# Kernel tuning notes

Hardware: AMD Instinct MI355X
Metric: run time of the kernel (lower is better)

Reference implementation:

```python
import math
import jax, jax.numpy as jnp
import numpy as np

B, S, H = 2, 2048, 1024
NH = 16
HD = H // NH  # 64
THETA = 10000.0


def _rope_cache(seq_len, head_dim, theta):
    inv_freq = 1.0 / (theta ** (jnp.arange(0, head_dim, 2, dtype=jnp.float32) / head_dim))
    pos = jnp.arange(seq_len, dtype=jnp.float32)
    freqs = jnp.outer(pos, inv_freq)           # (S, HD/2)
    emb = jnp.concatenate([freqs, freqs], -1)  # (S, HD)
    return jnp.cos(emb), jnp.sin(emb)


def _apply_rotary(x, cos, sin):
    # x: (B, NH, S, HD); cos/sin: (S, HD) broadcast over B, NH
    d = x.shape[-1] // 2
    x1, x2 = x[..., :d], x[..., d:]
    rotated = jnp.concatenate([-x2, x1], -1)
    return x * cos + rotated * sin


def setup_inputs() -> dict:
    key = jax.random.key(0)
    ks = jax.random.split(key, 5)
    scale = 1.0 / math.sqrt(H)
    return {
        'x': jax.random.normal(ks[0], (B, S, H), jnp.float32),
        'Wq': jax.random.normal(ks[1], (H, H), jnp.float32) * scale,
        'Wk': jax.random.normal(ks[2], (H, H), jnp.float32) * scale,
        'Wv': jax.random.normal(ks[3], (H, H), jnp.float32) * scale,
        'Wo': jax.random.normal(ks[4], (H, H), jnp.float32) * scale,
    }


def reference(x, Wq, Wk, Wv, Wo):
    b, s, h = x.shape
    # projections (nn.Linear: x @ W.T)
    q = (x @ Wq.T).reshape(b, s, NH, HD).transpose(0, 2, 1, 3)
    k = (x @ Wk.T).reshape(b, s, NH, HD).transpose(0, 2, 1, 3)
    v = (x @ Wv.T).reshape(b, s, NH, HD).transpose(0, 2, 1, 3)
    cos, sin = _rope_cache(s, HD, THETA)
    q = _apply_rotary(q, cos, sin)
    k = _apply_rotary(k, cos, sin)
    scale = 1.0 / math.sqrt(HD)
    attn = jnp.einsum('bhqd,bhkd->bhqk', q, k) * scale
    causal = jnp.triu(jnp.ones((s, s), dtype=bool), k=1)
    attn = jnp.where(causal, -jnp.inf, attn)
    attn = jax.nn.softmax(attn, axis=-1)
    out = jnp.einsum('bhqk,bhkd->bhqd', attn, v)
    out = out.transpose(0, 2, 1, 3).reshape(b, s, h)
    return out @ Wo.T
```

## Files before the change

### kernel.cpp

```cpp
#include <hip/hip_runtime.h>

#define B_  2
#define S_  2048
#define H_  1024
#define NH_ 16
#define HD_ 64
#define M_  (B_ * S_)

typedef short  short8  __attribute__((ext_vector_type(8)));
typedef __bf16 bf16x8  __attribute__((ext_vector_type(8)));
typedef float  f32x4   __attribute__((ext_vector_type(4)));

__device__ __forceinline__ ushort f2bf(float f) {
  union { float f; unsigned u; } v; v.f = f;
  unsigned r = v.u + 0x7fffu + ((v.u >> 16) & 1u);
  return (ushort)(r >> 16);
}
__device__ __forceinline__ float bf2f(ushort u) {
  union { unsigned u; float f; } v; v.u = ((unsigned)u) << 16;
  return v.f;
}
__device__ __forceinline__ unsigned cvtpk(float lo, float hi) {
  unsigned r;
  asm("v_cvt_pk_bf16_f32 %0, %1, %2" : "=v"(r) : "v"(lo), "v"(hi));
  return r;
}

__device__ __forceinline__ void gload_lds16(const void* g, void* l) {
  __builtin_amdgcn_global_load_lds(
      (const __attribute__((address_space(1))) void*)g,
      (__attribute__((address_space(3))) void*)l, 16, 0, 0);
}

__device__ __forceinline__ f32x4 mfma_bf16(short8 a, short8 b, f32x4 c) {
  return __builtin_amdgcn_mfma_f32_16x16x32_bf16(
      __builtin_bit_cast(bf16x8, a), __builtin_bit_cast(bf16x8, b), c, 0, 0, 0);
}

__device__ __forceinline__ int swzK(int r, int c) {
  return r * 64 + ((c ^ (r & 7)) << 3);
}
__device__ __forceinline__ int swzV(int r, int c) {
  return r * 128 + ((c ^ (r & 7)) << 3);
}

__device__ __forceinline__ float redmax64(float a) {
  a = fmaxf(a, __shfl_xor(a, 16));
  a = fmaxf(a, __shfl_xor(a, 32));
  return a;
}

__global__ __launch_bounds__(256)
void prep(const float* __restrict__ x, const float* __restrict__ Wq,
          const float* __restrict__ Wk, const float* __restrict__ Wv,
          const float* __restrict__ Wo, ushort* __restrict__ xb,
          ushort* __restrict__ Wqkv, ushort* __restrict__ Wob,
          float* __restrict__ ct, float* __restrict__ st) {
  int bid = blockIdx.x, t = threadIdx.x;
  if (bid < 4096) {
    int i = (bid * 256 + t) * 4;
    float4 v = *(const float4*)&x[i];
    ushort4 o;
    o.x = f2bf(v.x); o.y = f2bf(v.y); o.z = f2bf(v.z); o.w = f2bf(v.w);
    *(ushort4*)&xb[i] = o;
  } else if (bid < 8192) {
    int y = (bid - 4096) >> 10;
    const float* src = (y == 0) ? Wq : (y == 1) ? Wk : (y == 2) ? Wv : Wo;
    ushort* dst = (y == 3) ? Wob : Wqkv + (size_t)y * H_ * H_;
    int i = (((bid - 4096) & 1023) * 256 + t) * 4;
    float4 v = *(const float4*)&src[i];
    ushort4 o;
    o.x = f2bf(v.x); o.y = f2bf(v.y); o.z = f2bf(v.z); o.w = f2bf(v.w);
    *(ushort4*)&dst[i] = o;
  } else {
    int i = (bid - 8192) * 256 + t;
    int pos = i >> 5, d2 = i & 31;
    float invf = powf(10000.0f, -(float)d2 / 32.0f);
    float fr = (float)pos * invf;
    ct[i] = cosf(fr);
    st[i] = sinf(fr);
  }
}

template <int OUT_BF16>
__global__ __launch_bounds__(256)
void gemm_bt(const ushort* __restrict__ A, const ushort* __restrict__ Bm,
             void* __restrict__ Cout, int Mdim, int Ndim, int Kdim) {
  __shared__ ushort As[128 * 64];
  __shared__ ushort Bs[128 * 64];
  int t = threadIdx.x;
  int w = t >> 6, l = t & 63;
  int m0 = blockIdx.y * 128, n0 = blockIdx.x * 128;
  int wr = (w >> 1) * 64, wc = (w & 1) * 64;
  int lrow = l & 15, g = l >> 4;

  f32x4 acc[4][4];
#pragma unroll
  for (int mi = 0; mi < 4; ++mi)
#pragma unroll
    for (int ni = 0; ni < 4; ++ni) acc[mi][ni] = f32x4{0.f, 0.f, 0.f, 0.f};

  for (int k0 = 0; k0 < Kdim; k0 += 64) {
    __syncthreads();
#pragma unroll
    for (int cc = 0; cc < 4; ++cc) {
      int slot = cc * 256 + t;
      int r = slot >> 3, c = slot & 7;
      int cs = (c ^ (r & 7)) << 3;
      gload_lds16(&A[(size_t)(m0 + r) * Kdim + k0 + cs], &As[slot * 8]);
      gload_lds16(&Bm[(size_t)(n0 + r) * Kdim + k0 + cs], &Bs[slot * 8]);
    }
    __syncthreads();
#pragma unroll
    for (int kk = 0; kk < 2; ++kk) {
      short8 af[4], bfr[4];
#pragma unroll
      for (int i = 0; i < 4; ++i)
        af[i] = *(const short8*)&As[swzK(wr + i * 16 + lrow, kk * 4 + g)];
#pragma unroll
      for (int i = 0; i < 4; ++i)
        bfr[i] = *(const short8*)&Bs[swzK(wc + i * 16 + lrow, kk * 4 + g)];
#pragma unroll
      for (int mi = 0; mi < 4; ++mi)
#pragma unroll
        for (int ni = 0; ni < 4; ++ni)
          acc[mi][ni] = mfma_bf16(af[mi], bfr[ni], acc[mi][ni]);
    }
  }

#pragma unroll
  for (int mi = 0; mi < 4; ++mi)
#pragma unroll
    for (int ni = 0; ni < 4; ++ni)
#pragma unroll
      for (int j = 0; j < 4; ++j) {
        int row = m0 + wr + mi * 16 + g * 4 + j;
        int col = n0 + wc + ni * 16 + lrow;
        float vv = acc[mi][ni][j];
        if (OUT_BF16)
          ((ushort*)Cout)[(size_t)row * Ndim + col] = f2bf(vv);
        else
          ((float*)Cout)[(size_t)row * Ndim + col] = vv;
      }
}

__global__ __launch_bounds__(256)
void rope_scatter(const ushort* __restrict__ QKV, const float* __restrict__ ct,
                  const float* __restrict__ st, ushort* __restrict__ qb,
                  ushort* __restrict__ kb) {
  const float SC = 0.125f * 1.44269504f;
  int i = blockIdx.x * 256 + threadIdx.x;
  int row = i >> 9;
  int rem = i & 511;
  int h = rem >> 5, d2 = rem & 31;
  int b = row >> 11, s = row & 2047;
  size_t base = (size_t)row * 3072;
  float c = ct[s * 32 + d2], sn = st[s * 32 + d2];
  size_t o = ((size_t)(b * NH_ + h) * S_ + s) * HD_;

  float x1 = bf2f(QKV[base + h * 64 + d2]);
  float x2 = bf2f(QKV[base + h * 64 + d2 + 32]);
  qb[o + d2]      = f2bf((x1 * c - x2 * sn) * SC);
  qb[o + d2 + 32] = f2bf((x2 * c + x1 * sn) * SC);

  x1 = bf2f(QKV[base + 1024 + h * 64 + d2]);
  x2 = bf2f(QKV[base + 1024 + h * 64 + d2 + 32]);
  kb[o + d2]      = f2bf(x1 * c - x2 * sn);
  kb[o + d2 + 32] = f2bf(x2 * c + x1 * sn);
}

__global__ __launch_bounds__(256)
void transp_v(const ushort* __restrict__ QKV, ushort* __restrict__ vt) {
  __shared__ ushort T[64][72];
  int s0 = blockIdx.x * 64, bh = blockIdx.y;
  int b = bh >> 4, h = bh & 15;
  int t = threadIdx.x;
#pragma unroll
  for (int cc = 0; cc < 2; ++cc) {
    int slot = cc * 256 + t;
    int r = slot >> 3, c = slot & 7;
    short8 v = *(const short8*)
        &QKV[(size_t)(b * S_ + s0 + r) * 3072 + 2048 + h * 64 + c * 8];
#pragma unroll
    for (int i = 0; i < 8; ++i) T[c * 8 + i][r] = (ushort)v[i];
  }
  __syncthreads();
  ushort* dst = vt + (size_t)bh * HD_ * S_;
#pragma unroll
  for (int cc = 0; cc < 2; ++cc) {
    int slot = cc * 256 + t;
    int d = slot >> 3, c = slot & 7;
    *(short8*)&dst[(size_t)d * S_ + s0 + c * 8] = *(const short8*)&T[d][c * 8];
  }
}

__global__ __launch_bounds__(512, 4)
void flash_attn(const ushort* __restrict__ qb, const ushort* __restrict__ kb,
                const ushort* __restrict__ vt, ushort* __restrict__ ctx) {
  __shared__ ushort Ks[128 * 64];
  __shared__ ushort Vs[2][64 * 128];
  __shared__ ushort Ps[128 * 64];
  int bh = blockIdx.y;
  int qt = (blockIdx.y & 16) ? (int)blockIdx.x : (15 - (int)blockIdx.x);
  int b = bh >> 4, h = bh & 15;
  int t = threadIdx.x, w = t >> 6, l = t & 63;
  int lrow = l & 15, g = l >> 4;
  int wrow = w * 16;
  const ushort* Q = qb + (size_t)bh * S_ * HD_;
  const ushort* K = kb + (size_t)bh * S_ * HD_;
  const ushort* V = vt + (size_t)bh * HD_ * S_;

  short8 ones;
#pragma unroll
  for (int i = 0; i < 8; ++i) ones[i] = (short)0x3F80;

#pragma unroll
  for (int cc = 0; cc < 2; ++cc) {
    int slot = cc * 512 + t;
    int r = slot >> 3, c = slot & 7;
    int cs = (c ^ (r & 7)) << 3;
    gload_lds16(&K[(size_t)r * 64 + cs], &Ks[slot * 8]);
  }
#pragma unroll
  for (int cc = 0; cc < 2; ++cc) {
    int slot = cc * 512 + t;
    int r = slot >> 4, c = slot & 15;
    int cs = (c ^ (r & 7)) << 3;
    gload_lds16(&V[(size_t)r * S_ + cs], &Vs[0][slot * 8]);
  }
  short8 aq[2];
  {
    int qrow = qt * 128 + wrow + lrow;
#pragma unroll
    for (int ks = 0; ks < 2; ++ks)
      aq[ks] = *(const short8*)&Q[(size_t)qrow * 64 + ks * 32 + g * 8];
  }
  __syncthreads();

  float m_ = -1e30f, ls_ = 0.f;
  f32x4 O[4];
#pragma unroll
  for (int nf = 0; nf < 4; ++nf) O[nf] = f32x4{0.f, 0.f, 0.f, 0.f};

  int nkt = qt + 1;
  for (int kt = 0; kt < nkt; ++kt) {
    const ushort* Vc = Vs[kt & 1];

    f32x4 sc[8];
#pragma unroll
    for (int nf = 0; nf < 8; ++nf) sc[nf] = f32x4{0.f, 0.f, 0.f, 0.f};
    __builtin_amdgcn_s_setprio(1);
#pragma unroll
    for (int ks = 0; ks < 2; ++ks)
#pragma unroll
      for (int nf = 0; nf < 8; ++nf) {
        short8 bk = *(const short8*)&Ks[swzK(nf * 16 + lrow, ks * 4 + g)];
        sc[nf] = mfma_bf16(bk, aq[ks], sc[nf]);
      }
    __builtin_amdgcn_s_setprio(0);

    __syncthreads();

    if (kt + 1 < nkt) {
      int nb = (kt + 1) & 1;
#pragma unroll
      for (int cc = 0; cc < 2; ++cc) {
        int slot = cc * 512 + t;
        int r = slot >> 3, c = slot & 7;
        int cs = (c ^ (r & 7)) << 3;
        gload_lds16(&K[(size_t)((kt + 1) * 128 + r) * 64 + cs], &Ks[slot * 8]);
      }
#pragma unroll
      for (int cc = 0; cc < 2; ++cc) {
        int slot = cc * 512 + t;
        int r = slot >> 4, c = slot & 15;
        int cs = (c ^ (r & 7)) << 3;
        gload_lds16(&V[(size_t)r * S_ + (kt + 1) * 128 + cs], &Vs[nb][slot * 8]);
      }
    }

    int qbase = qt * 128 + wrow;
    if (kt * 128 + 127 > qbase) {
      int qi = qbase + lrow;
#pragma unroll
      for (int nf = 0; nf < 8; ++nf) {
        int kbase = kt * 128 + nf * 16 + g * 4;
#pragma unroll
        for (int j = 0; j < 4; ++j)
          if (kbase + j > qi) sc[nf][j] = -1e30f;
      }
    }

    f32x4 v4 = sc[0];
#pragma unroll
    for (int nf = 1; nf < 8; ++nf)
#pragma unroll
      for (int j = 0; j < 4; ++j) v4[j] = fmaxf(v4[j], sc[nf][j]);
    float mx = redmax64(fmaxf(fmaxf(v4[0], v4[1]), fmaxf(v4[2], v4[3])));

    bool nor = __all(mx <= m_ + 8.f);
    if (!nor) {
      float mnew = fmaxf(m_, mx);
      float al = exp2f(m_ - mnew);
      m_ = mnew;
      ls_ *= al;
#pragma unroll
      for (int nf = 0; nf < 4; ++nf)
#pragma unroll
        for (int j = 0; j < 4; ++j) O[nf][j] *= al;
    }

#pragma unroll
    for (int nf = 0; nf < 8; ++nf)
#pragma unroll
      for (int j = 0; j < 4; ++j) sc[nf][j] = exp2f(sc[nf][j] - m_);

    f32x4 sacc = f32x4{0.f, 0.f, 0.f, 0.f};
#pragma unroll
    for (int half = 0; half < 2; ++half) {
      int prow = wrow + lrow;
#pragma unroll
      for (int nf2 = 0; nf2 < 4; ++nf2) {
        int nf = half * 4 + nf2;
        uint2 pk;
        pk.x = cvtpk(sc[nf][0], sc[nf][1]);
        pk.y = cvtpk(sc[nf][2], sc[nf][3]);
        *(uint2*)&Ps[swzK(prow, nf2 * 2 + (g >> 1)) + (g & 1) * 4] = pk;
      }
      __builtin_amdgcn_s_setprio(1);
#pragma unroll
      for (int ks2 = 0; ks2 < 2; ++ks2) {
        short8 ap = *(const short8*)&Ps[swzK(wrow + lrow, ks2 * 4 + g)];
        sacc = mfma_bf16(ones, ap, sacc);
#pragma unroll
        for (int nf = 0; nf < 4; ++nf) {
          short8 bv = *(const short8*)&Vc[swzV(nf * 16 + lrow, half * 8 + ks2 * 4 + g)];
          O[nf] = mfma_bf16(bv, ap, O[nf]);
        }
      }
      __builtin_amdgcn_s_setprio(0);
    }
    ls_ += sacc[0];

    __syncthreads();
  }

  float inv = 1.f / ls_;
  int srow = qt * 128 + wrow + lrow;
#pragma unroll
  for (int nf = 0; nf < 4; ++nf) {
    uint2 pk;
    pk.x = cvtpk(O[nf][0] * inv, O[nf][1] * inv);
    pk.y = cvtpk(O[nf][2] * inv, O[nf][3] * inv);
    *(uint2*)&ctx[((size_t)b * S_ + srow) * H_ + h * 64 + nf * 16 + g * 4] = pk;
  }
}

extern "C" void kernel_launch(void* const* d_in, const int* in_sizes, int n_in,
                              void* d_out, int out_size, void* d_ws, size_t ws_size,
                              hipStream_t stream) {
  const float* x  = (const float*)d_in[0];
  const float* Wq = (const float*)d_in[1];
  const float* Wk = (const float*)d_in[2];
  const float* Wv = (const float*)d_in[3];
  const float* Wo = (const float*)d_in[4];

  char* ws = (char*)d_ws;
  size_t off = 0;
  ushort* xb   = (ushort*)(ws + off); off += (size_t)M_ * H_ * 2;
  ushort* Wqkv = (ushort*)(ws + off); off += (size_t)3 * H_ * H_ * 2;
  ushort* Wob  = (ushort*)(ws + off); off += (size_t)H_ * H_ * 2;
  float*  ct   = (float*)(ws + off);  off += (size_t)S_ * 32 * 4;
  float*  st   = (float*)(ws + off);  off += (size_t)S_ * 32 * 4;
  ushort* QKV  = (ushort*)(ws + off); off += (size_t)M_ * 3 * H_ * 2;
  ushort* qb   = (ushort*)(ws + off); off += (size_t)M_ * H_ * 2;
  ushort* kb   = (ushort*)(ws + off); off += (size_t)M_ * H_ * 2;
  ushort* vtb  = (ushort*)(ws + off); off += (size_t)M_ * H_ * 2;
  ushort* ctx  = (ushort*)(ws + off); off += (size_t)M_ * H_ * 2;

  prep<<<8448, 256, 0, stream>>>(x, Wq, Wk, Wv, Wo, xb, Wqkv, Wob, ct, st);

  gemm_bt<1><<<dim3(3 * H_ / 128, M_ / 128), 256, 0, stream>>>(
      xb, Wqkv, QKV, M_, 3 * H_, H_);
  rope_scatter<<<M_ * NH_ * 32 / 256, 256, 0, stream>>>(QKV, ct, st, qb, kb);
  transp_v<<<dim3(S_ / 64, B_ * NH_), 256, 0, stream>>>(QKV, vtb);
  flash_attn<<<dim3(S_ / 128, B_ * NH_), 512, 0, stream>>>(qb, kb, vtb, ctx);
  gemm_bt<0><<<dim3(H_ / 128, M_ / 128), 256, 0, stream>>>(
      ctx, Wob, d_out, M_, H_, H_);
}
```

Baseline: 122.2 us.

## Fuse RoPE, Q/K head scatter and V transpose into QKV GEMM epilogue

```diff
diff --git a/kernel.cpp b/kernel.cpp
--- a/kernel.cpp
+++ b/kernel.cpp
@@ -82,10 +82,13 @@
   }
 }
 
-template <int OUT_BF16>
+template <int MODE>
 __global__ __launch_bounds__(256)
 void gemm_bt(const ushort* __restrict__ A, const ushort* __restrict__ Bm,
-             void* __restrict__ Cout, int Mdim, int Ndim, int Kdim) {
+             void* __restrict__ Cout, int Mdim, int Ndim, int Kdim,
+             const float* __restrict__ ct, const float* __restrict__ st,
+             ushort* __restrict__ qb, ushort* __restrict__ kb,
+             ushort* __restrict__ vt) {
   __shared__ ushort As[128 * 64];
   __shared__ ushort Bs[128 * 64];
   int t = threadIdx.x;
@@ -128,69 +131,56 @@
     }
   }
 
-#pragma unroll
-  for (int mi = 0; mi < 4; ++mi)
-#pragma unroll
-    for (int ni = 0; ni < 4; ++ni)
-#pragma unroll
-      for (int j = 0; j < 4; ++j) {
-        int row = m0 + wr + mi * 16 + g * 4 + j;
-        int col = n0 + wc + ni * 16 + lrow;
-        float vv = acc[mi][ni][j];
-        if (OUT_BF16)
-          ((ushort*)Cout)[(size_t)row * Ndim + col] = f2bf(vv);
-        else
-          ((float*)Cout)[(size_t)row * Ndim + col] = vv;
-      }
-}
-
-__global__ __launch_bounds__(256)
-void rope_scatter(const ushort* __restrict__ QKV, const float* __restrict__ ct,
-                  const float* __restrict__ st, ushort* __restrict__ qb,
-                  ushort* __restrict__ kb) {
-  const float SC = 0.125f * 1.44269504f;
-  int i = blockIdx.x * 256 + threadIdx.x;
-  int row = i >> 9;
-  int rem = i & 511;
-  int h = rem >> 5, d2 = rem & 31;
-  int b = row >> 11, s = row & 2047;
-  size_t base = (size_t)row * 3072;
-  float c = ct[s * 32 + d2], sn = st[s * 32 + d2];
-  size_t o = ((size_t)(b * NH_ + h) * S_ + s) * HD_;
-
-  float x1 = bf2f(QKV[base + h * 64 + d2]);
-  float x2 = bf2f(QKV[base + h * 64 + d2 + 32]);
-  qb[o + d2]      = f2bf((x1 * c - x2 * sn) * SC);
-  qb[o + d2 + 32] = f2bf((x2 * c + x1 * sn) * SC);
-
-  x1 = bf2f(QKV[base + 1024 + h * 64 + d2]);
-  x2 = bf2f(QKV[base + 1024 + h * 64 + d2 + 32]);
-  kb[o + d2]      = f2bf(x1 * c - x2 * sn);
-  kb[o + d2 + 32] = f2bf(x2 * c + x1 * sn);
-}
-
-__global__ __launch_bounds__(256)
-void transp_v(const ushort* __restrict__ QKV, ushort* __restrict__ vt) {
-  __shared__ ushort T[64][72];
-  int s0 = blockIdx.x * 64, bh = blockIdx.y;
-  int b = bh >> 4, h = bh & 15;
-  int t = threadIdx.x;
-#pragma unroll
-  for (int cc = 0; cc < 2; ++cc) {
-    int slot = cc * 256 + t;
-    int r = slot >> 3, c = slot & 7;
-    short8 v = *(const short8*)
-        &QKV[(size_t)(b * S_ + s0 + r) * 3072 + 2048 + h * 64 + c * 8];
-#pragma unroll
-    for (int i = 0; i < 8; ++i) T[c * 8 + i][r] = (ushort)v[i];
-  }
-  __syncthreads();
-  ushort* dst = vt + (size_t)bh * HD_ * S_;
-#pragma unroll
-  for (int cc = 0; cc < 2; ++cc) {
-    int slot = cc * 256 + t;
-    int d = slot >> 3, c = slot & 7;
-    *(short8*)&dst[(size_t)d * S_ + s0 + c * 8] = *(const short8*)&T[d][c * 8];
+  if (MODE == 0) {
+#pragma unroll
+    for (int mi = 0; mi < 4; ++mi)
+#pragma unroll
+      for (int ni = 0; ni < 4; ++ni)
+#pragma unroll
+        for (int j = 0; j < 4; ++j) {
+          int row = m0 + wr + mi * 16 + g * 4 + j;
+          int col = n0 + wc + ni * 16 + lrow;
+          ((float*)Cout)[(size_t)row * Ndim + col] = acc[mi][ni][j];
+        }
+  } else {
+    int colbase = n0 + wc;
+    int sector = colbase >> 10;
+    int h = (colbase & 1023) >> 6;
+    if (sector < 2) {
+      ushort* dst = (sector == 0) ? qb : kb;
+      const float SCq = (sector == 0) ? 0.125f * 1.44269504f : 1.0f;
+#pragma unroll
+      for (int mi = 0; mi < 4; ++mi)
+#pragma unroll
+        for (int j = 0; j < 4; ++j) {
+          int row = m0 + wr + mi * 16 + g * 4 + j;
+          int b = row >> 11, s = row & 2047;
+          size_t o = ((size_t)(b * NH_ + h) * S_ + s) * HD_;
+          float c0 = ct[s * 32 + lrow],      s0 = st[s * 32 + lrow];
+          float c1 = ct[s * 32 + 16 + lrow], s1 = st[s * 32 + 16 + lrow];
+          float x1a = acc[mi][0][j], x2a = acc[mi][2][j];
+          float x1b = acc[mi][1][j], x2b = acc[mi][3][j];
+          dst[o + lrow]      = f2bf((x1a * c0 - x2a * s0) * SCq);
+          dst[o + lrow + 32] = f2bf((x2a * c0 + x1a * s0) * SCq);
+          dst[o + lrow + 16] = f2bf((x1b * c1 - x2b * s1) * SCq);
+          dst[o + lrow + 48] = f2bf((x2b * c1 + x1b * s1) * SCq);
+        }
+    } else {
+#pragma unroll
+      for (int mi = 0; mi < 4; ++mi) {
+        int row0 = m0 + wr + mi * 16 + g * 4;
+        int b = row0 >> 11, s0r = row0 & 2047;
+        size_t obase = (size_t)(b * NH_ + h) * HD_ * S_;
+#pragma unroll
+        for (int ni = 0; ni < 4; ++ni) {
+          int d = ni * 16 + lrow;
+          uint2 pk;
+          pk.x = cvtpk(acc[mi][ni][0], acc[mi][ni][1]);
+          pk.y = cvtpk(acc[mi][ni][2], acc[mi][ni][3]);
+          *(uint2*)&vt[obase + (size_t)d * S_ + s0r] = pk;
+        }
+      }
+    }
   }
 }
 
@@ -372,7 +362,6 @@
   ushort* Wob  = (ushort*)(ws + off); off += (size_t)H_ * H_ * 2;
   float*  ct   = (float*)(ws + off);  off += (size_t)S_ * 32 * 4;
   float*  st   = (float*)(ws + off);  off += (size_t)S_ * 32 * 4;
-  ushort* QKV  = (ushort*)(ws + off); off += (size_t)M_ * 3 * H_ * 2;
   ushort* qb   = (ushort*)(ws + off); off += (size_t)M_ * H_ * 2;
   ushort* kb   = (ushort*)(ws + off); off += (size_t)M_ * H_ * 2;
   ushort* vtb  = (ushort*)(ws + off); off += (size_t)M_ * H_ * 2;
@@ -380,11 +369,9 @@
 
   prep<<<8448, 256, 0, stream>>>(x, Wq, Wk, Wv, Wo, xb, Wqkv, Wob, ct, st);
 
-  gemm_bt<1><<<dim3(3 * H_ / 128, M_ / 128), 256, 0, stream>>>(
-      xb, Wqkv, QKV, M_, 3 * H_, H_);
-  rope_scatter<<<M_ * NH_ * 32 / 256, 256, 0, stream>>>(QKV, ct, st, qb, kb);
-  transp_v<<<dim3(S_ / 64, B_ * NH_), 256, 0, stream>>>(QKV, vtb);
+  gemm_bt<2><<<dim3(3 * H_ / 128, M_ / 128), 256, 0, stream>>>(
+      xb, Wqkv, nullptr, M_, 3 * H_, H_, ct, st, qb, kb, vtb);
   flash_attn<<<dim3(S_ / 128, B_ * NH_), 512, 0, stream>>>(qb, kb, vtb, ctx);
   gemm_bt<0><<<dim3(H_ / 128, M_ / 128), 256, 0, stream>>>(
-      ctx, Wob, d_out, M_, H_, H_);
-}
+      ctx, Wob, d_out, M_, H_, H_, nullptr, nullptr, nullptr, nullptr, nullptr);
+}
```

After: 120.4 us. No clear change (-1.5%).
